# Kernel optimization log

Hardware: AMD Instinct MI355X
Metric: run time of the kernel (lower is better)

Reference implementation:

```python
import jax, jax.numpy as jnp
import numpy as np

U, I, D, L, NNZ, B = 100000, 50000, 64, 3, 3200000, 4096
N = U + I
MOMENTUM = 0.05

def setup_inputs() -> dict:
    key = jax.random.key(0)
    ks = jax.random.split(key, 10)
    return {
        'user_emb': jax.random.normal(ks[0], (U, D), jnp.float32) * 0.02,
        'item_emb': jax.random.normal(ks[1], (I, D), jnp.float32) * 0.02,
        'W': jax.random.normal(ks[2], (D, D), jnp.float32) * (1.0 / np.sqrt(D)),
        'b': jnp.zeros((D,), jnp.float32),
        'adj_rows': jax.random.randint(ks[3], (NNZ,), 0, N, jnp.int32),
        'adj_cols': jax.random.randint(ks[4], (NNZ,), 0, N, jnp.int32),
        'adj_vals': jax.random.uniform(ks[5], (NNZ,), jnp.float32) * 0.05,
        'users': jax.random.randint(ks[6], (B,), 0, U, jnp.int32),
        'items': jax.random.randint(ks[7], (B,), 0, I, jnp.int32),
        'u_his': jax.random.normal(ks[8], (U, D), jnp.float32),
        'i_his': jax.random.normal(ks[9], (I, D), jnp.float32),
    }

def _spmm(rows, cols, vals, x):
    # y = A @ x for sparse COO A: gather source rows, scale, scatter-add to dest rows
    return jax.ops.segment_sum(vals[:, None] * x[cols], rows, num_segments=N)

def reference(user_emb, item_emb, W, b, adj_rows, adj_cols, adj_vals, users, items, u_his, i_his):
    ego = jnp.concatenate([user_emb, item_emb], axis=0)  # [N, D]
    acc = ego
    cur = ego
    for _ in range(L):
        cur = _spmm(adj_rows, adj_cols, adj_vals, cur)
        acc = acc + cur
    all_emb = acc / (L + 1)           # mean over stacked layers
    u_all = all_emb[:U]
    i_all = all_emb[U:]
    u_online = u_all[users]           # [B, D]
    i_online = i_all[items]
    m = MOMENTUM
    u_target = jax.lax.stop_gradient(u_his[users] * m + u_online * (1.0 - m))
    i_target = jax.lax.stop_gradient(i_his[items] * m + i_online * (1.0 - m))
    p_u = u_online @ W.T + b
    p_i = i_online @ W.T + b
    return (p_u, u_target, p_i, i_target)
```

## Files before the change

kernel.cpp:

```cpp
#include <hip/hip_runtime.h>
#include <hip/hip_bf16.h>

#define U_CNT   100000
#define I_CNT   50000
#define D_DIM   64
#define N_NODES 150000
#define NNZ_E   3200000
#define B_SZ    4096

#define NSUB 1172
#define CAP2 4096
#define NPART 8
#define CAPP 512
#define TILE_E 8192
#define N_TILES ((NNZ_E + TILE_E - 1) / TILE_E)

#define CONV_THREADS (N_NODES * 16)
#define CONV_PER_BLK (512 * 4)
#define CONV_BLOCKS ((CONV_THREADS + CONV_PER_BLK - 1) / CONV_PER_BLK)

typedef unsigned int uint;
typedef unsigned short ushort_t;
typedef _Float16 half_t;
typedef half_t half2_t __attribute__((ext_vector_type(2)));

union h2u_t { uint u; half2_t h; };
__device__ __forceinline__ half2_t u2h2(uint u) { h2u_t c; c.u = u; return c.h; }
__device__ __forceinline__ uint h22u(half2_t h) { h2u_t c; c.h = h; return c.u; }
__device__ __forceinline__ half2_t h2shfl_xor(half2_t v, int m) {
    h2u_t c; c.h = v; c.u = (uint)__shfl_xor((int)c.u, m, 64); return c.h;
}
__device__ __forceinline__ float h2lo(uint u) { return (float)u2h2(u)[0]; }
__device__ __forceinline__ float h2hi(uint u) { return (float)u2h2(u)[1]; }

__global__ __launch_bounds__(512) void scatter_kernel(const int* __restrict__ rows,
                                                      const int* __restrict__ cols,
                                                      const float* __restrict__ vals,
                                                      int* __restrict__ pcursor,
                                                      int2* __restrict__ pmeta,
                                                      const float4* __restrict__ ue4,
                                                      const float4* __restrict__ ie4,
                                                      uint2* __restrict__ e2) {
    int tid = threadIdx.x;

    if (blockIdx.x >= N_TILES) {
        int g0 = (blockIdx.x - N_TILES) * CONV_PER_BLK + tid;
        #pragma unroll
        for (int k = 0; k < 4; ++k) {
            int g = g0 + k * 512;
            if (g < CONV_THREADS) {
                float4 f = (g < U_CNT * 16) ? ue4[g] : ie4[g - U_CNT * 16];
                half2_t a = { (half_t)f.x, (half_t)f.y };
                half2_t b = { (half_t)f.z, (half_t)f.w };
                uint2 o; o.x = h22u(a); o.y = h22u(b);
                e2[g] = o;
            }
        }
        return;
    }

    __shared__ int lcnt[NSUB];
    __shared__ int gofs[NSUB];
    int part = blockIdx.x & (NPART - 1);

    for (int i = tid; i < NSUB; i += 512) lcnt[i] = 0;
    __syncthreads();

    int base = blockIdx.x * TILE_E;
    int nk = NNZ_E - base - tid;
    nk = (nk <= 0) ? 0 : (nk + 511) >> 9;

    int pk[16]; float vv[16]; int sb[16]; int rk[16];
    #pragma unroll
    for (int k = 0; k < 16; ++k) {
        if (k < nk) {
            int j = base + tid + (k << 9);
            int r = rows[j];
            int c = cols[j];
            vv[k] = vals[j];
            sb[k] = r >> 7;
            pk[k] = ((r & 127) << 18) | c;
            rk[k] = atomicAdd(&lcnt[sb[k]], 1);
        }
    }
    __syncthreads();

    for (int i = tid; i < NSUB; i += 512) {
        int c = lcnt[i];
        gofs[i] = (c > 0) ? atomicAdd(&pcursor[part * NSUB + i], c) : 0;
    }
    __syncthreads();

    #pragma unroll
    for (int k = 0; k < 16; ++k) {
        if (k < nk) {
            int cellpos = gofs[sb[k]] + rk[k];
            if (cellpos < CAPP)
                pmeta[((size_t)(part * NSUB + sb[k])) * CAPP + cellpos] =
                    make_int2(pk[k], __float_as_int(vv[k]));
        }
    }
}

__global__ __launch_bounds__(512) void sort_spmm_kernel(const int* __restrict__ pcursor,
                                                        const int2* __restrict__ pmeta,
                                                        int2* __restrict__ meta2,
                                                        int* __restrict__ rstart,
                                                        int* __restrict__ rend,
                                                        const ushort_t* __restrict__ x,
                                                        ushort_t* __restrict__ out) {
    __shared__ int2 stage[CAP2];
    __shared__ int rcnt[128];
    __shared__ int rs[128];
    __shared__ int re_[128];
    __shared__ int cur[128];
    int g = blockIdx.x;
    int base = g * CAP2;
    int tid = threadIdx.x;
    int r0 = g << 7;

    int cnt_p[NPART], pfx[NPART];
    int cnt = 0;
    #pragma unroll
    for (int p = 0; p < NPART; ++p) {
        int c = pcursor[p * NSUB + g];
        if (c > CAPP) c = CAPP;
        cnt_p[p] = c; pfx[p] = cnt; cnt += c;
    }

    if (tid < 128) rcnt[tid] = 0;
    __syncthreads();

    #pragma unroll
    for (int p = 0; p < NPART; ++p) {
        const int2* seg = &pmeta[((size_t)(p * NSUB + g)) * CAPP];
        for (int i = tid; i < cnt_p[p]; i += 512) {
            int2 e = seg[i];
            stage[pfx[p] + i] = e;
            atomicAdd(&rcnt[((uint)e.x >> 18) & 127], 1);
        }
    }
    __syncthreads();

    if (tid < 64) {
        int c0 = rcnt[2 * tid], c1 = rcnt[2 * tid + 1];
        int s2 = c0 + c1, incl = s2;
        #pragma unroll
        for (int off = 1; off < 64; off <<= 1) {
            int t = __shfl_up(incl, off, 64);
            if (tid >= off) incl += t;
        }
        int s0 = incl - s2, s1 = incl - c1;
        rs[2 * tid] = s0;      re_[2 * tid] = s0 + c0;     cur[2 * tid] = s0;
        rs[2 * tid + 1] = s1;  re_[2 * tid + 1] = incl;    cur[2 * tid + 1] = s1;
        int r = r0 + 2 * tid;
        if (r < N_NODES)     { rstart[r]     = base + s0; rend[r]     = base + s0 + c0; }
        if (r + 1 < N_NODES) { rstart[r + 1] = base + s1; rend[r + 1] = base + incl;    }
    }
    __syncthreads();

    for (int i = tid; i < cnt; i += 512) {
        int2 e = stage[i];
        int rl = ((uint)e.x >> 18) & 127;
        int pos = atomicAdd(&cur[rl], 1);
        float v = __int_as_float(e.y);
        half2_t hv = { (half_t)v, (half_t)v };
        meta2[base + pos] = make_int2(e.x & 0x3FFFF, (int)h22u(hv));
    }
    __syncthreads();

    for (int i = tid; i < cnt; i += 512) stage[i] = meta2[base + i];
    __syncthreads();

    int wv   = tid >> 6;
    int lane = tid & 63;
    int sub  = lane >> 3;
    int l8   = lane & 7;
    const uint4* x4 = (const uint4*)x;

    for (int rr = 0; rr < 16; ++rr) {
        int rl = (wv << 4) + rr;
        int s = rs[rl], e = re_[rl];
        half2_t a0 = { (half_t)0, (half_t)0 };
        half2_t a1 = a0, a2 = a0, a3 = a0;

        if (e > s) {
            int last = e - 1;
            auto ldl = [&](int jj) -> int2 {
                int2 c = stage[jj < e ? jj : last];
                if (jj >= e) c.y = 0;
                return c;
            };
            int j = s + sub;
            int2 c0 = ldl(j);
            int2 c1 = ldl(j + 8);
            int2 c2 = ldl(j + 16);
            int2 c3 = ldl(j + 24);
            for (; j < e; j += 32) {
                uint4 x0 = x4[(size_t)(c0.x & 0x3FFFF) * 8 + l8];
                uint4 x1 = x4[(size_t)(c1.x & 0x3FFFF) * 8 + l8];
                uint4 x2 = x4[(size_t)(c2.x & 0x3FFFF) * 8 + l8];
                uint4 x3 = x4[(size_t)(c3.x & 0x3FFFF) * 8 + l8];
                int jn = j + 32;
                int2 n0 = ldl(jn);
                int2 n1 = ldl(jn + 8);
                int2 n2 = ldl(jn + 16);
                int2 n3 = ldl(jn + 24);
                half2_t v0 = u2h2((uint)c0.y);
                a0 += u2h2(x0.x) * v0; a1 += u2h2(x0.y) * v0;
                a2 += u2h2(x0.z) * v0; a3 += u2h2(x0.w) * v0;
                half2_t v1 = u2h2((uint)c1.y);
                a0 += u2h2(x1.x) * v1; a1 += u2h2(x1.y) * v1;
                a2 += u2h2(x1.z) * v1; a3 += u2h2(x1.w) * v1;
                half2_t v2 = u2h2((uint)c2.y);
                a0 += u2h2(x2.x) * v2; a1 += u2h2(x2.y) * v2;
                a2 += u2h2(x2.z) * v2; a3 += u2h2(x2.w) * v2;
                half2_t v3 = u2h2((uint)c3.y);
                a0 += u2h2(x3.x) * v3; a1 += u2h2(x3.y) * v3;
                a2 += u2h2(x3.z) * v3; a3 += u2h2(x3.w) * v3;
                c0 = n0; c1 = n1; c2 = n2; c3 = n3;
            }
        }
        a0 += h2shfl_xor(a0, 8);  a1 += h2shfl_xor(a1, 8);
        a2 += h2shfl_xor(a2, 8);  a3 += h2shfl_xor(a3, 8);
        a0 += h2shfl_xor(a0, 16); a1 += h2shfl_xor(a1, 16);
        a2 += h2shfl_xor(a2, 16); a3 += h2shfl_xor(a3, 16);
        a0 += h2shfl_xor(a0, 32); a1 += h2shfl_xor(a1, 32);
        a2 += h2shfl_xor(a2, 32); a3 += h2shfl_xor(a3, 32);

        int wid = r0 + rl;
        if (sub == 0 && wid < N_NODES) {
            uint4 r;
            r.x = h22u(a0); r.y = h22u(a1); r.z = h22u(a2); r.w = h22u(a3);
            ((uint4*)out)[(size_t)wid * 8 + l8] = r;
        }
    }
}

__global__ __launch_bounds__(256) void spmm_fp16_kernel(const int* __restrict__ rstart,
                                                        const int* __restrict__ rend,
                                                        const int2* __restrict__ csr,
                                                        const ushort_t* __restrict__ x,
                                                        ushort_t* __restrict__ out) {
    int gw   = (blockIdx.x * blockDim.x + threadIdx.x) >> 6;
    int lane = threadIdx.x & 63;
    int sub  = lane >> 3;
    int l8   = lane & 7;
    int wid0 = gw * 2, wid1 = gw * 2 + 1;
    if (wid0 >= N_NODES) return;
    const uint4* x4 = (const uint4*)x;

    int s0 = rstart[wid0], e0 = rend[wid0];
    int s1 = 0, e1 = 0;
    if (wid1 < N_NODES) { s1 = rstart[wid1]; e1 = rend[wid1]; }
    int last0 = (e0 - 1 < s0) ? s0 : e0 - 1;
    int last1 = (e1 - 1 < s1) ? s1 : e1 - 1;

    auto ld0 = [&](int jj) -> int2 {
        int2 c = csr[jj < e0 ? jj : last0];
        if (jj >= e0) c.y = 0;
        return c;
    };
    auto ld1 = [&](int jj) -> int2 {
        int2 c = csr[jj < e1 ? jj : last1];
        if (jj >= e1) c.y = 0;
        return c;
    };

    half2_t z = { (half_t)0, (half_t)0 };
    half2_t a00 = z, a01 = z, a02 = z, a03 = z;
    half2_t a10 = z, a11 = z, a12 = z, a13 = z;

    int j0 = s0 + sub, j1 = s1 + sub;
    int2 c00 = ld0(j0), c01 = ld0(j0 + 8), c02 = ld0(j0 + 16), c03 = ld0(j0 + 24);
    int2 c10 = ld1(j1), c11 = ld1(j1 + 8), c12 = ld1(j1 + 16), c13 = ld1(j1 + 24);
    while (j0 < e0 || j1 < e1) {
        uint4 x00 = x4[(size_t)(c00.x & 0x3FFFF) * 8 + l8];
        uint4 x01 = x4[(size_t)(c01.x & 0x3FFFF) * 8 + l8];
        uint4 x02 = x4[(size_t)(c02.x & 0x3FFFF) * 8 + l8];
        uint4 x03 = x4[(size_t)(c03.x & 0x3FFFF) * 8 + l8];
        uint4 x10 = x4[(size_t)(c10.x & 0x3FFFF) * 8 + l8];
        uint4 x11 = x4[(size_t)(c11.x & 0x3FFFF) * 8 + l8];
        uint4 x12 = x4[(size_t)(c12.x & 0x3FFFF) * 8 + l8];
        uint4 x13 = x4[(size_t)(c13.x & 0x3FFFF) * 8 + l8];
        int jn0 = j0 + 32, jn1 = j1 + 32;
        int2 n00 = ld0(jn0), n01 = ld0(jn0 + 8), n02 = ld0(jn0 + 16), n03 = ld0(jn0 + 24);
        int2 n10 = ld1(jn1), n11 = ld1(jn1 + 8), n12 = ld1(jn1 + 16), n13 = ld1(jn1 + 24);

        half2_t v;
        v = u2h2((uint)c00.y);
        a00 += u2h2(x00.x) * v; a01 += u2h2(x00.y) * v;
        a02 += u2h2(x00.z) * v; a03 += u2h2(x00.w) * v;
        v = u2h2((uint)c10.y);
        a10 += u2h2(x10.x) * v; a11 += u2h2(x10.y) * v;
        a12 += u2h2(x10.z) * v; a13 += u2h2(x10.w) * v;
        v = u2h2((uint)c01.y);
        a00 += u2h2(x01.x) * v; a01 += u2h2(x01.y) * v;
        a02 += u2h2(x01.z) * v; a03 += u2h2(x01.w) * v;
        v = u2h2((uint)c11.y);
        a10 += u2h2(x11.x) * v; a11 += u2h2(x11.y) * v;
        a12 += u2h2(x11.z) * v; a13 += u2h2(x11.w) * v;
        v = u2h2((uint)c02.y);
        a00 += u2h2(x02.x) * v; a01 += u2h2(x02.y) * v;
        a02 += u2h2(x02.z) * v; a03 += u2h2(x02.w) * v;
        v = u2h2((uint)c12.y);
        a10 += u2h2(x12.x) * v; a11 += u2h2(x12.y) * v;
        a12 += u2h2(x12.z) * v; a13 += u2h2(x12.w) * v;
        v = u2h2((uint)c03.y);
        a00 += u2h2(x03.x) * v; a01 += u2h2(x03.y) * v;
        a02 += u2h2(x03.z) * v; a03 += u2h2(x03.w) * v;
        v = u2h2((uint)c13.y);
        a10 += u2h2(x13.x) * v; a11 += u2h2(x13.y) * v;
        a12 += u2h2(x13.z) * v; a13 += u2h2(x13.w) * v;

        c00 = n00; c01 = n01; c02 = n02; c03 = n03;
        c10 = n10; c11 = n11; c12 = n12; c13 = n13;
        j0 = jn0; j1 = jn1;
    }
    a00 += h2shfl_xor(a00, 8);  a01 += h2shfl_xor(a01, 8);
    a02 += h2shfl_xor(a02, 8);  a03 += h2shfl_xor(a03, 8);
    a10 += h2shfl_xor(a10, 8);  a11 += h2shfl_xor(a11, 8);
    a12 += h2shfl_xor(a12, 8);  a13 += h2shfl_xor(a13, 8);
    a00 += h2shfl_xor(a00, 16); a01 += h2shfl_xor(a01, 16);
    a02 += h2shfl_xor(a02, 16); a03 += h2shfl_xor(a03, 16);
    a10 += h2shfl_xor(a10, 16); a11 += h2shfl_xor(a11, 16);
    a12 += h2shfl_xor(a12, 16); a13 += h2shfl_xor(a13, 16);
    a00 += h2shfl_xor(a00, 32); a01 += h2shfl_xor(a01, 32);
    a02 += h2shfl_xor(a02, 32); a03 += h2shfl_xor(a03, 32);
    a10 += h2shfl_xor(a10, 32); a11 += h2shfl_xor(a11, 32);
    a12 += h2shfl_xor(a12, 32); a13 += h2shfl_xor(a13, 32);

    if (sub == 0) {
        uint4 r;
        r.x = h22u(a00); r.y = h22u(a01); r.z = h22u(a02); r.w = h22u(a03);
        ((uint4*)out)[(size_t)wid0 * 8 + l8] = r;
    }
    if (sub == 1 && wid1 < N_NODES) {
        uint4 r;
        r.x = h22u(a10); r.y = h22u(a11); r.z = h22u(a12); r.w = h22u(a13);
        ((uint4*)out)[(size_t)wid1 * 8 + l8] = r;
    }
}

__global__ __launch_bounds__(256) void epilogue_kernel(const int* __restrict__ users,
                                                       const int* __restrict__ items,
                                                       const int* __restrict__ rstart,
                                                       const int* __restrict__ rend,
                                                       const int2* __restrict__ csr,
                                                       const ushort_t* __restrict__ ebuf,
                                                       const ushort_t* __restrict__ buf1,
                                                       const ushort_t* __restrict__ buf2,
                                                       const float* __restrict__ u_his,
                                                       const float* __restrict__ i_his,
                                                       const float* __restrict__ W,
                                                       const float* __restrict__ bvec,
                                                       float* __restrict__ out) {
    __shared__ float Wt[D_DIM * 65];
    __shared__ float bsh[D_DIM];
    __shared__ float on_s[4][D_DIM];
    for (int t = threadIdx.x; t < D_DIM * D_DIM; t += blockDim.x) {
        int j = t >> 6, k = t & 63;
        Wt[k * 65 + j] = W[t];
    }
    if (threadIdx.x < D_DIM) bsh[threadIdx.x] = bvec[threadIdx.x];

    int wv   = threadIdx.x >> 6;
    int wid  = blockIdx.x * 4 + wv;
    int lane = threadIdx.x & 63;
    int sub  = lane >> 4;
    int l16  = lane & 15;

    bool is_user = (wid < B_SZ);
    int  samp = is_user ? wid : wid - B_SZ;
    int  idx  = is_user ? users[samp] : items[samp];
    int  row  = is_user ? idx : (U_CNT + idx);

    const float* his = is_user ? u_his : i_his;
    float hisv = his[(size_t)idx * D_DIM + lane];
    uint2 eg = make_uint2(0, 0), b1v = eg, b2v = eg;
    if (sub == 0) {
        eg  = ((const uint2*)ebuf)[(size_t)row * 16 + l16];
        b1v = ((const uint2*)buf1)[(size_t)row * 16 + l16];
        b2v = ((const uint2*)buf2)[(size_t)row * 16 + l16];
    }

    int s = rstart[row], e = rend[row];
    int last = e - 1; if (last < s) last = s;
    auto ld = [&](int jj) -> int2 {
        int2 c = csr[jj < e ? jj : last];
        if (jj >= e) c.y = 0;
        return c;
    };
    half2_t c0 = { (half_t)0, (half_t)0 };
    half2_t c1 = c0;
    int j = s + sub;
    int2 e0 = ld(j);
    int2 e1 = ld(j + 4);
    int2 e2 = ld(j + 8);
    int2 e3 = ld(j + 12);
    for (; j < e; j += 16) {
        uint2 x0 = ((const uint2*)buf2)[(size_t)(e0.x & 0x3FFFF) * 16 + l16];
        uint2 x1 = ((const uint2*)buf2)[(size_t)(e1.x & 0x3FFFF) * 16 + l16];
        uint2 x2 = ((const uint2*)buf2)[(size_t)(e2.x & 0x3FFFF) * 16 + l16];
        uint2 x3 = ((const uint2*)buf2)[(size_t)(e3.x & 0x3FFFF) * 16 + l16];
        int jn = j + 16;
        int2 n0 = ld(jn);
        int2 n1 = ld(jn + 4);
        int2 n2 = ld(jn + 8);
        int2 n3 = ld(jn + 12);
        half2_t v0 = u2h2((uint)e0.y);
        c0 += u2h2(x0.x) * v0; c1 += u2h2(x0.y) * v0;
        half2_t v1 = u2h2((uint)e1.y);
        c0 += u2h2(x1.x) * v1; c1 += u2h2(x1.y) * v1;
        half2_t v2 = u2h2((uint)e2.y);
        c0 += u2h2(x2.x) * v2; c1 += u2h2(x2.y) * v2;
        half2_t v3 = u2h2((uint)e3.y);
        c0 += u2h2(x3.x) * v3; c1 += u2h2(x3.y) * v3;
        e0 = n0; e1 = n1; e2 = n2; e3 = n3;
    }
    c0 += h2shfl_xor(c0, 16); c1 += h2shfl_xor(c1, 16);
    c0 += h2shfl_xor(c0, 32); c1 += h2shfl_xor(c1, 32);

    if (sub == 0) {
        on_s[wv][l16 * 4 + 0] = (h2lo(eg.x) + h2lo(b1v.x) + h2lo(b2v.x) + (float)c0[0]) * 0.25f;
        on_s[wv][l16 * 4 + 1] = (h2hi(eg.x) + h2hi(b1v.x) + h2hi(b2v.x) + (float)c0[1]) * 0.25f;
        on_s[wv][l16 * 4 + 2] = (h2lo(eg.y) + h2lo(b1v.y) + h2lo(b2v.y) + (float)c1[0]) * 0.25f;
        on_s[wv][l16 * 4 + 3] = (h2hi(eg.y) + h2hi(b1v.y) + h2hi(b2v.y) + (float)c1[1]) * 0.25f;
    }
    __syncthreads();

    float online = on_s[wv][lane];
    float target = 0.05f * hisv + 0.95f * online;

    float p = bsh[lane];
    #pragma unroll
    for (int k = 0; k < D_DIM; ++k) {
        float ok = __shfl(online, k, 64);
        p = fmaf(ok, Wt[k * 65 + lane], p);
    }

    size_t base = is_user ? 0 : (size_t)2 * B_SZ * D_DIM;
    out[base + (size_t)samp * D_DIM + lane] = p;
    out[base + (size_t)B_SZ * D_DIM + (size_t)samp * D_DIM + lane] = target;
}


extern "C" void kernel_launch(void* const* d_in, const int* in_sizes, int n_in,
                              void* d_out, int out_size, void* d_ws, size_t ws_size,
                              hipStream_t stream) {
    const float* user_emb = (const float*)d_in[0];
    const float* item_emb = (const float*)d_in[1];
    const float* W        = (const float*)d_in[2];
    const float* bvec     = (const float*)d_in[3];
    const int*   adj_rows = (const int*)d_in[4];
    const int*   adj_cols = (const int*)d_in[5];
    const float* adj_vals = (const float*)d_in[6];
    const int*   users    = (const int*)d_in[7];
    const int*   items    = (const int*)d_in[8];
    const float* u_his    = (const float*)d_in[9];
    const float* i_his    = (const float*)d_in[10];
    float* out = (float*)d_out;

    char* ws = (char*)d_ws;
    size_t o = 0;
    ushort_t* ebuf  = (ushort_t*)(ws + o); o += (size_t)N_NODES * D_DIM * 2;
    ushort_t* buf1  = (ushort_t*)(ws + o); o += (size_t)N_NODES * D_DIM * 2;
    ushort_t* buf2  = (ushort_t*)(ws + o); o += (size_t)N_NODES * D_DIM * 2;
    int2*  pmeta    = (int2*)(ws + o);     o += (size_t)NPART * NSUB * CAPP * 8;
    int2*  meta2    = (int2*)(ws + o);     o += (size_t)NSUB * CAP2 * 8;
    int*   rstart   = (int*)(ws + o);      o += (size_t)N_NODES * 4;
    int*   rend     = (int*)(ws + o);      o += (size_t)N_NODES * 4;
    int*   pcursor  = (int*)(ws + o);      o += (size_t)NPART * NSUB * 4;
    (void)ws_size; (void)o; (void)in_sizes; (void)n_in; (void)out_size;

    hipMemsetAsync(pcursor, 0, (size_t)NPART * NSUB * 4, stream);

    scatter_kernel<<<N_TILES + CONV_BLOCKS, 512, 0, stream>>>(
        adj_rows, adj_cols, adj_vals, pcursor, pmeta,
        (const float4*)user_emb, (const float4*)item_emb, (uint2*)ebuf);

    sort_spmm_kernel<<<NSUB, 512, 0, stream>>>(pcursor, pmeta, meta2, rstart, rend,
                                               ebuf, buf1);

    int spmm_blocks = ((N_NODES + 1) / 2 + 3) / 4;
    spmm_fp16_kernel<<<spmm_blocks, 256, 0, stream>>>(rstart, rend, meta2, buf1, buf2);

    epilogue_kernel<<<(2 * B_SZ) / 4, 256, 0, stream>>>(users, items, rstart, rend, meta2,
                                                        ebuf, buf1, buf2,
                                                        u_his, i_his, W, bvec, out);
}
```

Measured before the change: 317.6 us.

## Place edges directly via atomic ranks and process two rows per wave iteration

```diff
diff --git a/kernel.cpp b/kernel.cpp
--- a/kernel.cpp
+++ b/kernel.cpp
@@ -113,31 +113,28 @@
     __shared__ int rcnt[128];
     __shared__ int rs[128];
     __shared__ int re_[128];
-    __shared__ int cur[128];
     int g = blockIdx.x;
     int base = g * CAP2;
     int tid = threadIdx.x;
     int r0 = g << 7;
 
-    int cnt_p[NPART], pfx[NPART];
-    int cnt = 0;
+    int cnt_p[NPART];
     #pragma unroll
     for (int p = 0; p < NPART; ++p) {
         int c = pcursor[p * NSUB + g];
-        if (c > CAPP) c = CAPP;
-        cnt_p[p] = c; pfx[p] = cnt; cnt += c;
+        cnt_p[p] = (c > CAPP) ? CAPP : c;
     }
 
     if (tid < 128) rcnt[tid] = 0;
     __syncthreads();
 
+    int2 ek[NPART]; int rk[NPART];
     #pragma unroll
     for (int p = 0; p < NPART; ++p) {
-        const int2* seg = &pmeta[((size_t)(p * NSUB + g)) * CAPP];
-        for (int i = tid; i < cnt_p[p]; i += 512) {
-            int2 e = seg[i];
-            stage[pfx[p] + i] = e;
-            atomicAdd(&rcnt[((uint)e.x >> 18) & 127], 1);
+        if (tid < cnt_p[p]) {
+            int2 e = pmeta[((size_t)(p * NSUB + g)) * CAPP + tid];
+            ek[p] = e;
+            rk[p] = atomicAdd(&rcnt[((uint)e.x >> 18) & 127], 1);
         }
     }
     __syncthreads();
@@ -151,25 +148,26 @@
             if (tid >= off) incl += t;
         }
         int s0 = incl - s2, s1 = incl - c1;
-        rs[2 * tid] = s0;      re_[2 * tid] = s0 + c0;     cur[2 * tid] = s0;
-        rs[2 * tid + 1] = s1;  re_[2 * tid + 1] = incl;    cur[2 * tid + 1] = s1;
+        rs[2 * tid] = s0;      re_[2 * tid] = s0 + c0;
+        rs[2 * tid + 1] = s1;  re_[2 * tid + 1] = incl;
         int r = r0 + 2 * tid;
         if (r < N_NODES)     { rstart[r]     = base + s0; rend[r]     = base + s0 + c0; }
         if (r + 1 < N_NODES) { rstart[r + 1] = base + s1; rend[r + 1] = base + incl;    }
     }
     __syncthreads();
 
-    for (int i = tid; i < cnt; i += 512) {
-        int2 e = stage[i];
-        int rl = ((uint)e.x >> 18) & 127;
-        int pos = atomicAdd(&cur[rl], 1);
-        float v = __int_as_float(e.y);
-        half2_t hv = { (half_t)v, (half_t)v };
-        meta2[base + pos] = make_int2(e.x & 0x3FFFF, (int)h22u(hv));
-    }
-    __syncthreads();
-
-    for (int i = tid; i < cnt; i += 512) stage[i] = meta2[base + i];
+    #pragma unroll
+    for (int p = 0; p < NPART; ++p) {
+        if (tid < cnt_p[p]) {
+            int rl = ((uint)ek[p].x >> 18) & 127;
+            int pos = rs[rl] + rk[p];
+            float v = __int_as_float(ek[p].y);
+            half2_t hv = { (half_t)v, (half_t)v };
+            int2 f = make_int2(ek[p].x & 0x3FFFF, (int)h22u(hv));
+            stage[pos] = f;
+            meta2[base + pos] = f;
+        }
+    }
     __syncthreads();
 
     int wv   = tid >> 6;
@@ -178,61 +176,98 @@
     int l8   = lane & 7;
     const uint4* x4 = (const uint4*)x;
 
-    for (int rr = 0; rr < 16; ++rr) {
-        int rl = (wv << 4) + rr;
-        int s = rs[rl], e = re_[rl];
-        half2_t a0 = { (half_t)0, (half_t)0 };
-        half2_t a1 = a0, a2 = a0, a3 = a0;
-
-        if (e > s) {
-            int last = e - 1;
-            auto ldl = [&](int jj) -> int2 {
-                int2 c = stage[jj < e ? jj : last];
-                if (jj >= e) c.y = 0;
-                return c;
-            };
-            int j = s + sub;
-            int2 c0 = ldl(j);
-            int2 c1 = ldl(j + 8);
-            int2 c2 = ldl(j + 16);
-            int2 c3 = ldl(j + 24);
-            for (; j < e; j += 32) {
-                uint4 x0 = x4[(size_t)(c0.x & 0x3FFFF) * 8 + l8];
-                uint4 x1 = x4[(size_t)(c1.x & 0x3FFFF) * 8 + l8];
-                uint4 x2 = x4[(size_t)(c2.x & 0x3FFFF) * 8 + l8];
-                uint4 x3 = x4[(size_t)(c3.x & 0x3FFFF) * 8 + l8];
-                int jn = j + 32;
-                int2 n0 = ldl(jn);
-                int2 n1 = ldl(jn + 8);
-                int2 n2 = ldl(jn + 16);
-                int2 n3 = ldl(jn + 24);
-                half2_t v0 = u2h2((uint)c0.y);
-                a0 += u2h2(x0.x) * v0; a1 += u2h2(x0.y) * v0;
-                a2 += u2h2(x0.z) * v0; a3 += u2h2(x0.w) * v0;
-                half2_t v1 = u2h2((uint)c1.y);
-                a0 += u2h2(x1.x) * v1; a1 += u2h2(x1.y) * v1;
-                a2 += u2h2(x1.z) * v1; a3 += u2h2(x1.w) * v1;
-                half2_t v2 = u2h2((uint)c2.y);
-                a0 += u2h2(x2.x) * v2; a1 += u2h2(x2.y) * v2;
-                a2 += u2h2(x2.z) * v2; a3 += u2h2(x2.w) * v2;
-                half2_t v3 = u2h2((uint)c3.y);
-                a0 += u2h2(x3.x) * v3; a1 += u2h2(x3.y) * v3;
-                a2 += u2h2(x3.z) * v3; a3 += u2h2(x3.w) * v3;
-                c0 = n0; c1 = n1; c2 = n2; c3 = n3;
-            }
-        }
-        a0 += h2shfl_xor(a0, 8);  a1 += h2shfl_xor(a1, 8);
-        a2 += h2shfl_xor(a2, 8);  a3 += h2shfl_xor(a3, 8);
-        a0 += h2shfl_xor(a0, 16); a1 += h2shfl_xor(a1, 16);
-        a2 += h2shfl_xor(a2, 16); a3 += h2shfl_xor(a3, 16);
-        a0 += h2shfl_xor(a0, 32); a1 += h2shfl_xor(a1, 32);
-        a2 += h2shfl_xor(a2, 32); a3 += h2shfl_xor(a3, 32);
-
-        int wid = r0 + rl;
-        if (sub == 0 && wid < N_NODES) {
+    for (int rp = 0; rp < 8; ++rp) {
+        int rl0 = (wv << 4) + rp * 2;
+        int rl1 = rl0 + 1;
+        int s0 = rs[rl0], e0 = re_[rl0];
+        int s1 = rs[rl1], e1 = re_[rl1];
+        int last0 = (e0 - 1 < s0) ? s0 : e0 - 1;
+        int last1 = (e1 - 1 < s1) ? s1 : e1 - 1;
+
+        auto ld0 = [&](int jj) -> int2 {
+            int2 c = stage[jj < e0 ? jj : last0];
+            if (jj >= e0) c.y = 0;
+            return c;
+        };
+        auto ld1 = [&](int jj) -> int2 {
+            int2 c = stage[jj < e1 ? jj : last1];
+            if (jj >= e1) c.y = 0;
+            return c;
+        };
+
+        half2_t z = { (half_t)0, (half_t)0 };
+        half2_t a00 = z, a01 = z, a02 = z, a03 = z;
+        half2_t a10 = z, a11 = z, a12 = z, a13 = z;
+
+        int j0 = s0 + sub, j1 = s1 + sub;
+        int2 c00 = ld0(j0), c01 = ld0(j0 + 8), c02 = ld0(j0 + 16), c03 = ld0(j0 + 24);
+        int2 c10 = ld1(j1), c11 = ld1(j1 + 8), c12 = ld1(j1 + 16), c13 = ld1(j1 + 24);
+        while (j0 < e0 || j1 < e1) {
+            uint4 x00 = x4[(size_t)(c00.x & 0x3FFFF) * 8 + l8];
+            uint4 x01 = x4[(size_t)(c01.x & 0x3FFFF) * 8 + l8];
+            uint4 x02 = x4[(size_t)(c02.x & 0x3FFFF) * 8 + l8];
+            uint4 x03 = x4[(size_t)(c03.x & 0x3FFFF) * 8 + l8];
+            uint4 x10 = x4[(size_t)(c10.x & 0x3FFFF) * 8 + l8];
+            uint4 x11 = x4[(size_t)(c11.x & 0x3FFFF) * 8 + l8];
+            uint4 x12 = x4[(size_t)(c12.x & 0x3FFFF) * 8 + l8];
+            uint4 x13 = x4[(size_t)(c13.x & 0x3FFFF) * 8 + l8];
+            int jn0 = j0 + 32, jn1 = j1 + 32;
+            int2 n00 = ld0(jn0), n01 = ld0(jn0 + 8), n02 = ld0(jn0 + 16), n03 = ld0(jn0 + 24);
+            int2 n10 = ld1(jn1), n11 = ld1(jn1 + 8), n12 = ld1(jn1 + 16), n13 = ld1(jn1 + 24);
+
+            half2_t v;
+            v = u2h2((uint)c00.y);
+            a00 += u2h2(x00.x) * v; a01 += u2h2(x00.y) * v;
+            a02 += u2h2(x00.z) * v; a03 += u2h2(x00.w) * v;
+            v = u2h2((uint)c10.y);
+            a10 += u2h2(x10.x) * v; a11 += u2h2(x10.y) * v;
+            a12 += u2h2(x10.z) * v; a13 += u2h2(x10.w) * v;
+            v = u2h2((uint)c01.y);
+            a00 += u2h2(x01.x) * v; a01 += u2h2(x01.y) * v;
+            a02 += u2h2(x01.z) * v; a03 += u2h2(x01.w) * v;
+            v = u2h2((uint)c11.y);
+            a10 += u2h2(x11.x) * v; a11 += u2h2(x11.y) * v;
+            a12 += u2h2(x11.z) * v; a13 += u2h2(x11.w) * v;
+            v = u2h2((uint)c02.y);
+            a00 += u2h2(x02.x) * v; a01 += u2h2(x02.y) * v;
+            a02 += u2h2(x02.z) * v; a03 += u2h2(x02.w) * v;
+            v = u2h2((uint)c12.y);
+            a10 += u2h2(x12.x) * v; a11 += u2h2(x12.y) * v;
+            a12 += u2h2(x12.z) * v; a13 += u2h2(x12.w) * v;
+            v = u2h2((uint)c03.y);
+            a00 += u2h2(x03.x) * v; a01 += u2h2(x03.y) * v;
+            a02 += u2h2(x03.z) * v; a03 += u2h2(x03.w) * v;
+            v = u2h2((uint)c13.y);
+            a10 += u2h2(x13.x) * v; a11 += u2h2(x13.y) * v;
+            a12 += u2h2(x13.z) * v; a13 += u2h2(x13.w) * v;
+
+            c00 = n00; c01 = n01; c02 = n02; c03 = n03;
+            c10 = n10; c11 = n11; c12 = n12; c13 = n13;
+            j0 = jn0; j1 = jn1;
+        }
+        a00 += h2shfl_xor(a00, 8);  a01 += h2shfl_xor(a01, 8);
+        a02 += h2shfl_xor(a02, 8);  a03 += h2shfl_xor(a03, 8);
+        a10 += h2shfl_xor(a10, 8);  a11 += h2shfl_xor(a11, 8);
+        a12 += h2shfl_xor(a12, 8);  a13 += h2shfl_xor(a13, 8);
+        a00 += h2shfl_xor(a00, 16); a01 += h2shfl_xor(a01, 16);
+        a02 += h2shfl_xor(a02, 16); a03 += h2shfl_xor(a03, 16);
+        a10 += h2shfl_xor(a10, 16); a11 += h2shfl_xor(a11, 16);
+        a12 += h2shfl_xor(a12, 16); a13 += h2shfl_xor(a13, 16);
+        a00 += h2shfl_xor(a00, 32); a01 += h2shfl_xor(a01, 32);
+        a02 += h2shfl_xor(a02, 32); a03 += h2shfl_xor(a03, 32);
+        a10 += h2shfl_xor(a10, 32); a11 += h2shfl_xor(a11, 32);
+        a12 += h2shfl_xor(a12, 32); a13 += h2shfl_xor(a13, 32);
+
+        int wid0 = r0 + rl0, wid1 = r0 + rl1;
+        if (sub == 0 && wid0 < N_NODES) {
             uint4 r;
-            r.x = h22u(a0); r.y = h22u(a1); r.z = h22u(a2); r.w = h22u(a3);
-            ((uint4*)out)[(size_t)wid * 8 + l8] = r;
+            r.x = h22u(a00); r.y = h22u(a01); r.z = h22u(a02); r.w = h22u(a03);
+            ((uint4*)out)[(size_t)wid0 * 8 + l8] = r;
+        }
+        if (sub == 1 && wid1 < N_NODES) {
+            uint4 r;
+            r.x = h22u(a10); r.y = h22u(a11); r.z = h22u(a12); r.w = h22u(a13);
+            ((uint4*)out)[(size_t)wid1 * 8 + l8] = r;
         }
     }
 }
```

Measured after the change: 311.4 us. No clear change (-2.0%).
